# Kernel tuning notes

Measured on AMD Instinct MI355X. Metric: run time of the kernel, lower is better.

Reference implementation:

```python
import jax, jax.numpy as jnp
import numpy as np

N_HOPS = 3
N_ENTITIES = 100000
EMB = 128
N_EDGES = 600000
N_REL = 64


def setup_inputs() -> dict:
    key = jax.random.key(0)
    k1, k2, k3, k4, k5, k6 = jax.random.split(key, 6)
    entity_emb = jax.random.normal(k1, (N_ENTITIES, EMB), dtype=jnp.float32)
    edge_emb = jax.random.normal(k2, (N_REL, EMB), dtype=jnp.float32)
    q_w = jax.random.normal(k3, (EMB, EMB), dtype=jnp.float32) * (1.0 / np.sqrt(EMB))
    k_w = jax.random.normal(k4, (EMB, EMB), dtype=jnp.float32) * (1.0 / np.sqrt(EMB))
    edge_index = jax.random.randint(k5, (2, N_EDGES), 0, N_ENTITIES, dtype=jnp.int64)
    edge_type = jax.random.randint(k6, (N_EDGES,), 0, N_REL, dtype=jnp.int64)
    return {
        "entity_emb": entity_emb,
        "edge_emb": edge_emb,
        "q_w": q_w,
        "k_w": k_w,
        "edge_index": edge_index,
        "edge_type": edge_type,
        "mess_dropout": 0,
    }


def reference(entity_emb, edge_emb, q_w, k_w, edge_index, edge_type, mess_dropout):
    head = edge_index[0]
    tail = edge_index[1]
    rel = edge_emb[edge_type]                       # [E, D] per-edge relation emb
    n = entity_emb.shape[0]

    agg = entity_emb
    out = jnp.zeros_like(entity_emb)
    for _ in range(N_HOPS):
        h = agg[head]                               # [E, D]
        t = agg[tail]                               # [E, D]
        left = h @ q_w                              # [E, D]
        right = jnp.tanh((rel * t) @ k_w)           # [E, D]
        att = jnp.sum(left * right, axis=1)         # [E]
        # scatter_softmax over destination (head) segments
        seg_max = jax.ops.segment_max(att, head, num_segments=n)
        e = jnp.exp(att - seg_max[head])
        seg_sum = jax.ops.segment_sum(e, head, num_segments=n)
        w = e / seg_sum[head]                       # [E]
        # weighted messages + scatter_mean by head
        msg = w[:, None] * rel * t                  # [E, D]
        summed = jax.ops.segment_sum(msg, head, num_segments=n)
        cnt = jax.ops.segment_sum(jnp.ones_like(att), head, num_segments=n)
        agg = summed / jnp.maximum(cnt, 1.0)[:, None]
        # mess_dropout disabled (mess_dropout == 0) -> deterministic
        # F.normalize: L2 row normalization with eps 1e-12
        norm = jnp.linalg.norm(agg, axis=1, keepdims=True)
        agg = agg / jnp.maximum(norm, 1e-12)
        out = out + agg + entity_emb
    return out
```

## Files before the change

kernel.cpp:

```cpp
#include <hip/hip_runtime.h>


#define DD 128
#define CAP1 96

typedef unsigned short u16;
typedef unsigned int u32;
typedef __attribute__((ext_vector_type(8))) __bf16 bf16x8;
typedef __attribute__((ext_vector_type(4))) float f32x4;

__device__ __forceinline__ float bf2f(u16 u) { return __uint_as_float(((u32)u) << 16); }
__device__ __forceinline__ u16 f2bf(float f) {
    u32 u = __float_as_uint(f);
    u += 0x7FFFu + ((u >> 16) & 1u);
    return (u16)(u >> 16);
}
__device__ __forceinline__ u32 cvt_pk_bf16(float a, float b) {
    u32 r;
    asm("v_cvt_pk_bf16_f32 %0, %1, %2" : "=v"(r) : "v"(a), "v"(b));
    return r;
}
__device__ __forceinline__ u32 mul_bf_bf(u32 a2, u32 b2) {
    float lo = bf2f((u16)(a2 & 0xffffu)) * bf2f((u16)(b2 & 0xffffu));
    float hi = bf2f((u16)(a2 >> 16)) * bf2f((u16)(b2 >> 16));
    return cvt_pk_bf16(lo, hi);
}
__device__ __forceinline__ float fast_tanh(float x) {
    float e = __builtin_amdgcn_exp2f(x * 2.8853900817779268f);
    float r = __builtin_amdgcn_rcpf(e + 1.f);
    return __builtin_fmaf(-2.f, r, 1.f);
}

__global__ void k_cvt(const float* __restrict__ src, u16* __restrict__ dst, int n8) {
    int i = blockIdx.x * blockDim.x + threadIdx.x;
    if (i >= n8) return;
    float4 a = ((const float4*)src)[i * 2];
    float4 b = ((const float4*)src)[i * 2 + 1];
    u32 pk[4] = {cvt_pk_bf16(a.x, a.y), cvt_pk_bf16(a.z, a.w),
                 cvt_pk_bf16(b.x, b.y), cvt_pk_bf16(b.z, b.w)};
    ((uint4*)dst)[i] = *(uint4*)pk;
}

__global__ void k_hist(const int* __restrict__ head, int E, int* __restrict__ counts) {
    int e = blockIdx.x * blockDim.x + threadIdx.x;
    if (e < E) atomicAdd(&counts[head[e]], 1);
}

__global__ void k_scan_a(const int* __restrict__ counts, int N, int* __restrict__ row_off,
                         int* __restrict__ partials) {
    __shared__ int sw[16];
    int i = blockIdx.x * 1024 + threadIdx.x;
    int v = (i < N) ? counts[i] : 0;
    int lane = threadIdx.x & 63, wid = threadIdx.x >> 6;
    int x = v;
    #pragma unroll
    for (int off = 1; off < 64; off <<= 1) {
        int t = __shfl_up(x, off);
        if (lane >= off) x += t;
    }
    if (lane == 63) sw[wid] = x;
    __syncthreads();
    if (threadIdx.x == 0) {
        int run = 0;
        for (int w0 = 0; w0 < 16; w0++) { int t = sw[w0]; sw[w0] = run; run += t; }
        partials[blockIdx.x] = run;
    }
    __syncthreads();
    if (i < N) row_off[i] = x - v + sw[wid];
}
__global__ void k_scan_b(int* __restrict__ partials, int nch) {
    if (blockIdx.x == 0 && threadIdx.x == 0) {
        int run = 0;
        for (int c = 0; c < nch; c++) { int t = partials[c]; partials[c] = run; run += t; }
    }
}
__global__ void k_scan_c(int* __restrict__ row_off, const int* __restrict__ partials, int N, int E) {
    int i = blockIdx.x * 1024 + threadIdx.x;
    if (i < N) row_off[i] += partials[blockIdx.x];
    if (i == 0) row_off[N] = E;
}
__global__ void k_fill(const int* __restrict__ head, const int* __restrict__ tail,
                       const int* __restrict__ etype, int E, const int* __restrict__ row_off,
                       int* __restrict__ cursor, int* __restrict__ c_head,
                       int* __restrict__ c_tail, int* __restrict__ c_type) {
    int e = blockIdx.x * blockDim.x + threadIdx.x;
    if (e >= E) return;
    int h = head[e];
    int p = row_off[h] + atomicAdd(&cursor[h], 1);
    c_head[p] = h; c_tail[p] = tail[e]; c_type[p] = etype[e];
}

__global__ void k_blk(const int* __restrict__ row_off, int N,
                      int* __restrict__ blk_n0, int* __restrict__ blk_n1) {
    int n = blockIdx.x * blockDim.x + threadIdx.x;
    if (n >= N) return;
    int b = row_off[n] / CAP1;
    atomicMin(&blk_n0[b], n);
    atomicMax(&blk_n1[b], n + 1);
}

__global__ void k_prep_swz(const float* __restrict__ src, u16* __restrict__ dst_swz) {
    int idx = blockIdx.x * 256 + threadIdx.x;
    if (idx >= DD * DD) return;
    int n = idx >> 7, k = idx & 127;
    float v = src[k * DD + n];
    int byte = (n * 256 + k * 2) ^ ((n & 7) << 4);
    dst_swz[byte >> 1] = f2bf(v);
}
__global__ void k_prep_plain(const float* __restrict__ src, u16* __restrict__ dst) {
    int idx = blockIdx.x * 256 + threadIdx.x;
    if (idx >= DD * DD) return;
    int n = idx >> 7, k = idx & 127;
    dst[n * DD + k] = f2bf(src[k * DD + n]);
}

__global__ void __launch_bounds__(256) k_qproj(const u16* __restrict__ aggb,
                                               const uint4* __restrict__ qwT_swz,
                                               u16* __restrict__ qh, int N) {
    __shared__ u16 sA[DD * DD];
    __shared__ u16 sB[DD * DD];
    int tid = threadIdx.x;
    {
        uint4* dst = (uint4*)sB;
        #pragma unroll
        for (int i = 0; i < 8; ++i) dst[i * 256 + tid] = qwT_swz[i * 256 + tid];
    }
    long base = (long)blockIdx.x * 128;
    int qq = tid & 3, er = tid >> 2;
    #pragma unroll
    for (int pass = 0; pass < 2; ++pass) {
        int rloc = pass * 64 + er;
        long n = base + rloc;
        int d0 = qq * 32;
        __align__(16) uint4 pk[4];
        if (n < N) {
            const uint4* ar = (const uint4*)(aggb + (size_t)n * DD + d0);
            #pragma unroll
            for (int c = 0; c < 4; ++c) pk[c] = ar[c];
        } else {
            #pragma unroll
            for (int c = 0; c < 4; ++c) pk[c] = (uint4){0u, 0u, 0u, 0u};
        }
        char* basep = (char*)sA;
        #pragma unroll
        for (int c = 0; c < 4; ++c) {
            int byte = (rloc * 256 + d0 * 2 + c * 16) ^ ((rloc & 7) << 4);
            *(uint4*)(basep + byte) = pk[c];
        }
    }
    __syncthreads();
    int lane = tid & 63, wid = tid >> 6;
    int lr = lane & 15, lg = lane >> 4;
    int rgbase = wid * 32;
    f32x4 acc[2][8];
    #pragma unroll
    for (int g = 0; g < 2; ++g)
        #pragma unroll
        for (int t = 0; t < 8; ++t) acc[g][t] = (f32x4){0.f, 0.f, 0.f, 0.f};
    const char* ab_ = (const char*)sA;
    const char* bb_ = (const char*)sB;
    int sw = (lr & 7) << 4;
    #pragma unroll
    for (int kc = 0; kc < 4; ++kc) {
        int koffb = kc * 64 + lg * 16;
        int r0 = rgbase + lr;
        bf16x8 a0 = *(const bf16x8*)(ab_ + ((r0 * 256 + koffb) ^ sw));
        bf16x8 a1 = *(const bf16x8*)(ab_ + (((r0 + 16) * 256 + koffb) ^ sw));
        #pragma unroll
        for (int t = 0; t < 8; ++t) {
            int n = t * 16 + lr;
            bf16x8 b = *(const bf16x8*)(bb_ + ((n * 256 + koffb) ^ sw));
            acc[0][t] = __builtin_amdgcn_mfma_f32_16x16x32_bf16(a0, b, acc[0][t], 0, 0, 0);
            acc[1][t] = __builtin_amdgcn_mfma_f32_16x16x32_bf16(a1, b, acc[1][t], 0, 0, 0);
        }
    }
    #pragma unroll
    for (int g = 0; g < 2; ++g)
        #pragma unroll
        for (int r = 0; r < 4; ++r) {
            long row = base + rgbase + g * 16 + lg * 4 + r;
            if (row < N) {
                u16* qrow = qh + (size_t)row * DD + lr;
                #pragma unroll
                for (int t = 0; t < 8; ++t) qrow[t * 16] = f2bf(acc[g][t][r]);
            }
        }
}

__global__ void __launch_bounds__(256, 4) k_fused(
        const u16* __restrict__ aggb, const u16* __restrict__ eembb,
        const u16* __restrict__ kwT, const u16* __restrict__ qh,
        const int* __restrict__ c_head, const int* __restrict__ c_tail,
        const int* __restrict__ c_type, const int* __restrict__ row_off,
        const int* __restrict__ blk_n0, const int* __restrict__ blk_n1,
        const float* __restrict__ entity,
        u16* __restrict__ aggb_next, float* __restrict__ outacc, int mode) {
    __shared__ u16 sX[DD * DD];
    __shared__ float satt[128];
    int n0 = blk_n0[blockIdx.x];
    if (n0 == 0x7f7f7f7f) return;
    int n1 = blk_n1[blockIdx.x];
    int p0 = row_off[n0];
    int span = min(row_off[n1] - p0, 128);
    int tid = threadIdx.x;
    int qq = tid & 3, er = tid >> 2;
    #pragma unroll
    for (int pass = 0; pass < 2; ++pass) {
        int eloc = pass * 64 + er;
        int d0 = qq * 32;
        __align__(16) u32 pk[16];
        if (eloc < span) {
            int p = p0 + eloc;
            int tl = c_tail[p], rl = c_type[p];
            const uint4* ar = (const uint4*)(aggb + (size_t)tl * DD + d0);
            const uint4* rr = (const uint4*)(eembb + (size_t)rl * DD + d0);
            #pragma unroll
            for (int c = 0; c < 4; ++c) {
                uint4 av = ar[c], rv = rr[c];
                pk[c * 4 + 0] = mul_bf_bf(av.x, rv.x);
                pk[c * 4 + 1] = mul_bf_bf(av.y, rv.y);
                pk[c * 4 + 2] = mul_bf_bf(av.z, rv.z);
                pk[c * 4 + 3] = mul_bf_bf(av.w, rv.w);
            }
        } else {
            #pragma unroll
            for (int i = 0; i < 16; ++i) pk[i] = 0u;
        }
        char* base = (char*)sX;
        #pragma unroll
        for (int c = 0; c < 4; ++c) {
            int byte = (eloc * 256 + d0 * 2 + c * 16) ^ ((eloc & 7) << 4);
            *(uint4*)(base + byte) = *(const uint4*)&pk[c * 4];
        }
    }
    __syncthreads();
    int lane = tid & 63, wid = tid >> 6;
    int lr = lane & 15, lg = lane >> 4;
    int egbase = wid * 32;
    const char* xb_ = (const char*)sX;
    int sw = (lr & 7) << 4;
    bf16x8 afrag[2][4];
    #pragma unroll
    for (int kc = 0; kc < 4; ++kc) {
        int koffb = kc * 64 + lg * 16;
        int r0 = egbase + lr;
        afrag[0][kc] = *(const bf16x8*)(xb_ + ((r0 * 256 + koffb) ^ sw));
        afrag[1][kc] = *(const bf16x8*)(xb_ + (((r0 + 16) * 256 + koffb) ^ sw));
    }
    int hh[8];
    #pragma unroll
    for (int g = 0; g < 2; ++g)
        #pragma unroll
        for (int r = 0; r < 4; ++r) {
            int eloc = egbase + g * 16 + lg * 4 + r;
            hh[g * 4 + r] = (eloc < span) ? c_head[p0 + eloc] : 0;
        }
    float attv[8] = {0.f, 0.f, 0.f, 0.f, 0.f, 0.f, 0.f, 0.f};
    #pragma unroll
    for (int t = 0; t < 8; ++t) {
        f32x4 acc0 = (f32x4){0.f, 0.f, 0.f, 0.f};
        f32x4 acc1 = (f32x4){0.f, 0.f, 0.f, 0.f};
        int n = t * 16 + lr;
        #pragma unroll
        for (int kc = 0; kc < 4; ++kc) {
            int koffe = kc * 32 + lg * 8;
            bf16x8 b = *(const bf16x8*)(kwT + n * DD + koffe);
            acc0 = __builtin_amdgcn_mfma_f32_16x16x32_bf16(afrag[0][kc], b, acc0, 0, 0, 0);
            acc1 = __builtin_amdgcn_mfma_f32_16x16x32_bf16(afrag[1][kc], b, acc1, 0, 0, 0);
        }
        #pragma unroll
        for (int r = 0; r < 4; ++r) {
            attv[r]     += fast_tanh(acc0[r]) * bf2f(qh[(size_t)hh[r] * DD + t * 16 + lr]);
            attv[4 + r] += fast_tanh(acc1[r]) * bf2f(qh[(size_t)hh[4 + r] * DD + t * 16 + lr]);
        }
    }
    #pragma unroll
    for (int off = 1; off < 16; off <<= 1) {
        #pragma unroll
        for (int i = 0; i < 8; ++i) attv[i] += __shfl_xor(attv[i], off);
    }
    if (lr == 0) {
        #pragma unroll
        for (int g = 0; g < 2; ++g)
            #pragma unroll
            for (int r = 0; r < 4; ++r) {
                int eloc = egbase + g * 16 + lg * 4 + r;
                if (eloc < span) satt[eloc] = attv[g * 4 + r];
            }
    }
    __syncthreads();
    for (int n = n0 + wid; n < n1; n += 4) {
        int s0 = row_off[n] - p0;
        int s1 = min(row_off[n + 1] - p0, 128);
        float a0 = 0.f, a1 = 0.f;
        if (s1 > s0) {
            float m = -1e30f;
            for (int p = s0; p < s1; ++p) m = fmaxf(m, satt[p]);
            for (int p = s0; p < s1; ++p) {
                float wgt = __expf(satt[p] - m);
                int byte = (p * 256 + lane * 4) ^ ((p & 7) << 4);
                u32 xv = *(const u32*)((const char*)sX + byte);
                a0 += wgt * bf2f((u16)(xv & 0xffffu));
                a1 += wgt * bf2f((u16)(xv >> 16));
            }
            float s = a0 * a0 + a1 * a1;
            #pragma unroll
            for (int off = 1; off < 64; off <<= 1) s += __shfl_xor(s, off);
            float sc = 1.f / fmaxf(sqrtf(s), 1e-12f);
            a0 *= sc; a1 *= sc;
        }
        size_t idx = (size_t)n * DD + lane * 2;
        *(u32*)(aggb_next + idx) = cvt_pk_bf16(a0, a1);
        float o0, o1;
        if (mode == 0) { o0 = a0; o1 = a1; }
        else { o0 = outacc[idx] + a0; o1 = outacc[idx + 1] + a1; }
        if (mode == 2) { o0 += 3.f * entity[idx]; o1 += 3.f * entity[idx + 1]; }
        outacc[idx] = o0; outacc[idx + 1] = o1;
    }
}

extern "C" void kernel_launch(void* const* d_in, const int* in_sizes, int n_in,
                              void* d_out, int out_size, void* d_ws, size_t ws_size,
                              hipStream_t stream) {
    const float* entity = (const float*)d_in[0];
    const float* eemb   = (const float*)d_in[1];
    const float* qw     = (const float*)d_in[2];
    const float* kw     = (const float*)d_in[3];
    const int*   eidx   = (const int*)d_in[4];
    const int*   etype  = (const int*)d_in[5];
    const int N = in_sizes[0] / DD;
    const int E = in_sizes[5];
    const int NREL = in_sizes[1] / DD;
    const int* head = eidx;
    const int* tail = eidx + E;
    const int NB = E / CAP1 + 2;

    char* w = (char*)d_ws;
    auto carve = [&](size_t bytes) -> void* {
        void* p = (void*)w;
        w += ((bytes + 255) / 256) * 256;
        return p;
    };
    u16* aggbA     = (u16*)carve((size_t)N * DD * 2);
    u16* aggbB     = (u16*)carve((size_t)N * DD * 2);
    u16* aggb0     = (u16*)carve((size_t)N * DD * 2);
    u16* qh        = (u16*)carve((size_t)N * DD * 2);
    u16* eembb     = (u16*)carve((size_t)NREL * DD * 2);
    int* counts    = (int*)carve((size_t)N * 4);
    int* row_off   = (int*)carve((size_t)(N + 1) * 4);
    int* cursor    = (int*)carve((size_t)N * 4);
    int* c_head    = (int*)carve((size_t)E * 4);
    int* c_tail    = (int*)carve((size_t)E * 4);
    int* c_type    = (int*)carve((size_t)E * 4);
    u16* qwT_swz   = (u16*)carve((size_t)DD * DD * 2);
    u16* kwT       = (u16*)carve((size_t)DD * DD * 2);
    int* blk_n0    = (int*)carve((size_t)NB * 4);
    int* blk_n1    = (int*)carve((size_t)NB * 4);
    int* partials  = (int*)carve(4096);
    (void)ws_size; (void)n_in; (void)out_size;

    hipMemsetAsync(counts, 0, (size_t)N * 4, stream);
    hipMemsetAsync(cursor, 0, (size_t)N * 4, stream);
    hipMemsetAsync(blk_n0, 0x7f, (size_t)NB * 4, stream);
    hipMemsetAsync(blk_n1, 0, (size_t)NB * 4, stream);
    k_prep_swz<<<(DD * DD + 255) / 256, 256, 0, stream>>>(qw, qwT_swz);
    k_prep_plain<<<(DD * DD + 255) / 256, 256, 0, stream>>>(kw, kwT);
    int n8 = N * DD / 8;
    k_cvt<<<(n8 + 255) / 256, 256, 0, stream>>>(entity, aggb0, n8);
    int r8 = NREL * DD / 8;
    k_cvt<<<(r8 + 255) / 256, 256, 0, stream>>>(eemb, eembb, r8);
    k_hist<<<(E + 255) / 256, 256, 0, stream>>>(head, E, counts);
    int nch = (N + 1023) / 1024;
    k_scan_a<<<nch, 1024, 0, stream>>>(counts, N, row_off, partials);
    k_scan_b<<<1, 64, 0, stream>>>(partials, nch);
    k_scan_c<<<nch, 1024, 0, stream>>>(row_off, partials, N, E);
    k_fill<<<(E + 255) / 256, 256, 0, stream>>>(head, tail, etype, E, row_off, cursor,
                                                c_head, c_tail, c_type);
    k_blk<<<(N + 255) / 256, 256, 0, stream>>>(row_off, N, blk_n0, blk_n1);

    const u16* cur = aggb0;
    u16* bufs[2] = {aggbA, aggbB};
    for (int hop = 0; hop < 3; hop++) {
        k_qproj<<<(N + 127) / 128, 256, 0, stream>>>(cur, (const uint4*)qwT_swz, qh, N);
        u16* nxt = bufs[hop & 1];
        int mode = (hop == 0) ? 0 : ((hop == 2) ? 2 : 1);
        k_fused<<<NB, 256, 0, stream>>>(cur, eembb, kwT, qh, c_head, c_tail, c_type,
                                        row_off, blk_n0, blk_n1, entity,
                                        nxt, (float*)d_out, mode);
        cur = nxt;
    }
}
```

Baseline: 647.9 us.

## Defer output accumulation to final kernel and batch qh gathers per half

Each hop's bf16 aggregate now goes to its own buffer, and the fp32 output read-modify-write that ran inside every fused hop kernel is removed. A single elementwise kernel at the end sums the three hop results plus three times the entity embedding. Separately, the per-t scattered 16-bit loads of qh for the attention dot product are grouped into per-half batches issued before the MFMA loop, so more loads are in flight at once. The cost is an extra workspace buffer and one extra launch, and the output now sums bf16-rounded aggregates instead of fp32 ones.

```diff
diff --git a/kernel.cpp b/kernel.cpp
--- a/kernel.cpp
+++ b/kernel.cpp
@@ -39,6 +39,32 @@
     u32 pk[4] = {cvt_pk_bf16(a.x, a.y), cvt_pk_bf16(a.z, a.w),
                  cvt_pk_bf16(b.x, b.y), cvt_pk_bf16(b.z, b.w)};
     ((uint4*)dst)[i] = *(uint4*)pk;
+}
+
+__global__ void k_out(const u16* __restrict__ a1, const u16* __restrict__ a2,
+                      const u16* __restrict__ a3, const float* __restrict__ entity,
+                      float* __restrict__ out, int n8) {
+    int i = blockIdx.x * blockDim.x + threadIdx.x;
+    if (i >= n8) return;
+    uint4 x1 = ((const uint4*)a1)[i];
+    uint4 x2 = ((const uint4*)a2)[i];
+    uint4 x3 = ((const uint4*)a3)[i];
+    float4 e0 = ((const float4*)entity)[i * 2];
+    float4 e1 = ((const float4*)entity)[i * 2 + 1];
+    float o[8];
+    const u32 xs1[4] = {x1.x, x1.y, x1.z, x1.w};
+    const u32 xs2[4] = {x2.x, x2.y, x2.z, x2.w};
+    const u32 xs3[4] = {x3.x, x3.y, x3.z, x3.w};
+    const float es[8] = {e0.x, e0.y, e0.z, e0.w, e1.x, e1.y, e1.z, e1.w};
+    #pragma unroll
+    for (int c = 0; c < 4; ++c) {
+        o[c * 2 + 0] = 3.f * es[c * 2 + 0] + bf2f((u16)(xs1[c] & 0xffffu)) +
+                       bf2f((u16)(xs2[c] & 0xffffu)) + bf2f((u16)(xs3[c] & 0xffffu));
+        o[c * 2 + 1] = 3.f * es[c * 2 + 1] + bf2f((u16)(xs1[c] >> 16)) +
+                       bf2f((u16)(xs2[c] >> 16)) + bf2f((u16)(xs3[c] >> 16));
+    }
+    ((float4*)out)[i * 2]     = *(float4*)&o[0];
+    ((float4*)out)[i * 2 + 1] = *(float4*)&o[4];
 }
 
 __global__ void k_hist(const int* __restrict__ head, int E, int* __restrict__ counts) {
@@ -193,8 +219,7 @@
         const int* __restrict__ c_head, const int* __restrict__ c_tail,
         const int* __restrict__ c_type, const int* __restrict__ row_off,
         const int* __restrict__ blk_n0, const int* __restrict__ blk_n1,
-        const float* __restrict__ entity,
-        u16* __restrict__ aggb_next, float* __restrict__ outacc, int mode) {
+        u16* __restrict__ aggb_next) {
     __shared__ u16 sX[DD * DD];
     __shared__ float satt[128];
     int n0 = blk_n0[blockIdx.x];
@@ -257,21 +282,40 @@
         }
     float attv[8] = {0.f, 0.f, 0.f, 0.f, 0.f, 0.f, 0.f, 0.f};
     #pragma unroll
-    for (int t = 0; t < 8; ++t) {
-        f32x4 acc0 = (f32x4){0.f, 0.f, 0.f, 0.f};
-        f32x4 acc1 = (f32x4){0.f, 0.f, 0.f, 0.f};
-        int n = t * 16 + lr;
-        #pragma unroll
-        for (int kc = 0; kc < 4; ++kc) {
-            int koffe = kc * 32 + lg * 8;
-            bf16x8 b = *(const bf16x8*)(kwT + n * DD + koffe);
-            acc0 = __builtin_amdgcn_mfma_f32_16x16x32_bf16(afrag[0][kc], b, acc0, 0, 0, 0);
-            acc1 = __builtin_amdgcn_mfma_f32_16x16x32_bf16(afrag[1][kc], b, acc1, 0, 0, 0);
-        }
-        #pragma unroll
-        for (int r = 0; r < 4; ++r) {
-            attv[r]     += fast_tanh(acc0[r]) * bf2f(qh[(size_t)hh[r] * DD + t * 16 + lr]);
-            attv[4 + r] += fast_tanh(acc1[r]) * bf2f(qh[(size_t)hh[4 + r] * DD + t * 16 + lr]);
+    for (int half = 0; half < 2; ++half) {
+        u32 qv[8][2];
+        #pragma unroll
+        for (int i = 0; i < 8; ++i) {
+            const u16* qr = qh + (size_t)hh[i] * DD + lr;
+            #pragma unroll
+            for (int tp = 0; tp < 2; ++tp) {
+                int t0 = half * 4 + tp * 2;
+                u16 a = qr[t0 * 16];
+                u16 b = qr[(t0 + 1) * 16];
+                qv[i][tp] = (u32)a | ((u32)b << 16);
+            }
+        }
+        #pragma unroll
+        for (int tt = 0; tt < 4; ++tt) {
+            int t = half * 4 + tt;
+            f32x4 acc0 = (f32x4){0.f, 0.f, 0.f, 0.f};
+            f32x4 acc1 = (f32x4){0.f, 0.f, 0.f, 0.f};
+            int n = t * 16 + lr;
+            #pragma unroll
+            for (int kc = 0; kc < 4; ++kc) {
+                int koffe = kc * 32 + lg * 8;
+                bf16x8 b = *(const bf16x8*)(kwT + n * DD + koffe);
+                acc0 = __builtin_amdgcn_mfma_f32_16x16x32_bf16(afrag[0][kc], b, acc0, 0, 0, 0);
+                acc1 = __builtin_amdgcn_mfma_f32_16x16x32_bf16(afrag[1][kc], b, acc1, 0, 0, 0);
+            }
+            #pragma unroll
+            for (int r = 0; r < 4; ++r) {
+                u32 q0 = qv[r][tt >> 1], q1 = qv[4 + r][tt >> 1];
+                u16 v0 = (tt & 1) ? (u16)(q0 >> 16) : (u16)(q0 & 0xffffu);
+                u16 v1 = (tt & 1) ? (u16)(q1 >> 16) : (u16)(q1 & 0xffffu);
+                attv[r]     += fast_tanh(acc0[r]) * bf2f(v0);
+                attv[4 + r] += fast_tanh(acc1[r]) * bf2f(v1);
+            }
         }
     }
     #pragma unroll
@@ -311,11 +355,6 @@
         }
         size_t idx = (size_t)n * DD + lane * 2;
         *(u32*)(aggb_next + idx) = cvt_pk_bf16(a0, a1);
-        float o0, o1;
-        if (mode == 0) { o0 = a0; o1 = a1; }
-        else { o0 = outacc[idx] + a0; o1 = outacc[idx + 1] + a1; }
-        if (mode == 2) { o0 += 3.f * entity[idx]; o1 += 3.f * entity[idx + 1]; }
-        outacc[idx] = o0; outacc[idx + 1] = o1;
     }
 }
 
@@ -341,9 +380,10 @@
         w += ((bytes + 255) / 256) * 256;
         return p;
     };
-    u16* aggbA     = (u16*)carve((size_t)N * DD * 2);
-    u16* aggbB     = (u16*)carve((size_t)N * DD * 2);
     u16* aggb0     = (u16*)carve((size_t)N * DD * 2);
+    u16* aggb1     = (u16*)carve((size_t)N * DD * 2);
+    u16* aggb2     = (u16*)carve((size_t)N * DD * 2);
+    u16* aggb3     = (u16*)carve((size_t)N * DD * 2);
     u16* qh        = (u16*)carve((size_t)N * DD * 2);
     u16* eembb     = (u16*)carve((size_t)NREL * DD * 2);
     int* counts    = (int*)carve((size_t)N * 4);
@@ -378,15 +418,14 @@
                                                 c_head, c_tail, c_type);
     k_blk<<<(N + 255) / 256, 256, 0, stream>>>(row_off, N, blk_n0, blk_n1);
 
+    u16* hops[3] = {aggb1, aggb2, aggb3};
     const u16* cur = aggb0;
-    u16* bufs[2] = {aggbA, aggbB};
     for (int hop = 0; hop < 3; hop++) {
         k_qproj<<<(N + 127) / 128, 256, 0, stream>>>(cur, (const uint4*)qwT_swz, qh, N);
-        u16* nxt = bufs[hop & 1];
-        int mode = (hop == 0) ? 0 : ((hop == 2) ? 2 : 1);
         k_fused<<<NB, 256, 0, stream>>>(cur, eembb, kwT, qh, c_head, c_tail, c_type,
-                                        row_off, blk_n0, blk_n1, entity,
-                                        nxt, (float*)d_out, mode);
-        cur = nxt;
-    }
-}
+                                        row_off, blk_n0, blk_n1, hops[hop]);
+        cur = hops[hop];
+    }
+    k_out<<<(n8 + 255) / 256, 256, 0, stream>>>(aggb1, aggb2, aggb3, entity,
+                                                (float*)d_out, n8);
+}
```

Result: slower. 760.6 us (+17.4%).
